# Performance work log

Hardware: AMD Instinct MI355X
Metric: run time of the kernel (lower is better)

The kernel has to match this reference:

```python
import jax, jax.numpy as jnp
import numpy as np

N = 4096          # nodes (single graph, batch=None)
E = 65536         # edges (avg degree 16)
C = 256           # hidden_channels
L = 3             # num_layers
H = 8             # attention heads
EPS = 1e-5        # batchnorm eps


def setup_inputs() -> dict:
    key = jax.random.key(0)
    ks = iter(jax.random.split(key, 64))
    s = 0.05
    d = {}
    d['x'] = jax.random.normal(next(ks), (N, 1), dtype=jnp.float32)
    d['edge_index'] = jax.random.randint(next(ks), (2, E), 0, N, dtype=jnp.int32)
    # input projection Linear(1, C)
    d['lin1_w'] = jax.random.normal(next(ks), (C, 1), dtype=jnp.float32) * s
    d['lin1_b'] = jnp.zeros((C,), dtype=jnp.float32)
    # GIN MLP: Linear(C,C) -> ReLU -> Linear(C,C), stacked over layers
    d['gin_w1'] = jax.random.normal(next(ks), (L, C, C), dtype=jnp.float32) * s
    d['gin_b1'] = jnp.zeros((L, C), dtype=jnp.float32)
    d['gin_w2'] = jax.random.normal(next(ks), (L, C, C), dtype=jnp.float32) * s
    d['gin_b2'] = jnp.zeros((L, C), dtype=jnp.float32)
    # MultiheadAttention projections
    for nm in ['attn_wq', 'attn_wk', 'attn_wv', 'attn_wo']:
        d[nm] = jax.random.normal(next(ks), (L, C, C), dtype=jnp.float32) * s
    for nm in ['attn_bq', 'attn_bk', 'attn_bv', 'attn_bo']:
        d[nm] = jnp.zeros((L, C), dtype=jnp.float32)
    # three BatchNorms per GPSConv layer
    for nm in ['bn1', 'bn2', 'bn3']:
        d[nm + '_g'] = jnp.ones((L, C), dtype=jnp.float32)
        d[nm + '_b'] = jnp.zeros((L, C), dtype=jnp.float32)
    # GPSConv feedforward: Linear(C, 2C) -> ReLU -> Linear(2C, C)
    d['mlp_w1'] = jax.random.normal(next(ks), (L, 2 * C, C), dtype=jnp.float32) * s
    d['mlp_b1'] = jnp.zeros((L, 2 * C), dtype=jnp.float32)
    d['mlp_w2'] = jax.random.normal(next(ks), (L, C, 2 * C), dtype=jnp.float32) * s
    d['mlp_b2'] = jnp.zeros((L, C), dtype=jnp.float32)
    return d


def _bn(v, g, b):
    # training-mode BatchNorm1d over the node dimension (biased variance)
    m = v.mean(0)
    var = v.var(0)
    return (v - m) * jax.lax.rsqrt(var + EPS) * g + b


def _gps_forward(x, edge_index, lin1_w, lin1_b, gin_w1, gin_b1, gin_w2, gin_b2,
                 attn_wq, attn_bq, attn_wk, attn_bk, attn_wv, attn_bv,
                 attn_wo, attn_bo, bn1_g, bn1_b, bn2_g, bn2_b, bn3_g, bn3_b,
                 mlp_w1, mlp_b1, mlp_w2, mlp_b2):
    h = x @ lin1_w.T + lin1_b                     # [N, C]
    src, dst = edge_index[0], edge_index[1]
    dh = C // H
    scale = 1.0 / jnp.sqrt(jnp.float32(dh))
    for l in range(L):
        xin = h
        # --- GIN branch: gather -> scatter-sum -> MLP ---
        agg = jax.ops.segment_sum(xin[src], dst, num_segments=N)   # [N, C]
        z = xin + agg                                               # eps=0
        z = jax.nn.relu(z @ gin_w1[l].T + gin_b1[l]) @ gin_w2[l].T + gin_b2[l]
        h1 = _bn(z + xin, bn1_g[l], bn1_b[l])
        # --- global multihead attention over all N nodes ---
        q = (xin @ attn_wq[l].T + attn_bq[l]).reshape(N, H, dh)
        k = (xin @ attn_wk[l].T + attn_bk[l]).reshape(N, H, dh)
        v = (xin @ attn_wv[l].T + attn_bv[l]).reshape(N, H, dh)
        scores = jnp.einsum('nhd,mhd->hnm', q, k) * scale           # [H, N, N]
        a = jax.nn.softmax(scores, axis=-1)
        o = jnp.einsum('hnm,mhd->nhd', a, v).reshape(N, C)
        o = o @ attn_wo[l].T + attn_bo[l]
        h2 = _bn(o + xin, bn2_g[l], bn2_b[l])
        # --- combine + feedforward ---
        s = h1 + h2
        m = jax.nn.relu(s @ mlp_w1[l].T + mlp_b1[l]) @ mlp_w2[l].T + mlp_b2[l]
        h = _bn(s + m, bn3_g[l], bn3_b[l])
    return h


def reference(x, edge_index, lin1_w, lin1_b, gin_w1, gin_b1, gin_w2, gin_b2,
              attn_wq, attn_bq, attn_wk, attn_bk, attn_wv, attn_bv,
              attn_wo, attn_bo, bn1_g, bn1_b, bn2_g, bn2_b, bn3_g, bn3_b,
              mlp_w1, mlp_b1, mlp_w2, mlp_b2):
    return _gps_forward(x, edge_index, lin1_w, lin1_b, gin_w1, gin_b1, gin_w2,
                        gin_b2, attn_wq, attn_bq, attn_wk, attn_bk, attn_wv,
                        attn_bv, attn_wo, attn_bo, bn1_g, bn1_b, bn2_g, bn2_b,
                        bn3_g, bn3_b, mlp_w1, mlp_b1, mlp_w2, mlp_b2)
```

## Files before the change

kernel.cpp:

```cpp
#include <hip/hip_runtime.h>

#define NN 4096
#define NE 65536
#define C 256
#define NL 3
#define NH 8
#define DH 32
#define EPS 1e-5f
#define SPLIT 4
#define KT8 (NN/128/SPLIT)
#define SR 512
#define ATTN_BLKS ((NN/128)*NH*SPLIT)
#define VS 136

typedef __bf16 bf16x8 __attribute__((ext_vector_type(8)));
typedef __bf16 bf16x4v __attribute__((ext_vector_type(4)));
typedef float f32x4 __attribute__((ext_vector_type(4)));
typedef short bf16x4s __attribute__((ext_vector_type(4)));

#define QSCALE (0.17677669529663687f * 1.4426950408889634f)

#define CC1 (C*C)
#define GS 72

__global__ __launch_bounds__(256) void prep_w(const float* __restrict__ s0,
        const float* __restrict__ s1, const float* __restrict__ s2,
        const float* __restrict__ s3, const float* __restrict__ s4,
        const float* __restrict__ s5, const float* __restrict__ s6,
        const float* __restrict__ s7, __bf16* __restrict__ dst) {
    int g = blockIdx.y;
    int i = (blockIdx.x*256 + threadIdx.x)*4;
    const float* src; int n;
    switch (g) {
        case 0: src=s0; n=3*CC1; break;
        case 1: src=s1; n=3*CC1; break;
        case 2: src=s2; n=3*CC1; break;
        case 3: src=s3; n=3*CC1; break;
        case 4: src=s4; n=3*CC1; break;
        case 5: src=s5; n=3*CC1; break;
        case 6: src=s6; n=6*CC1; break;
        default: src=s7; n=6*CC1; break;
    }
    if (i >= n) return;
    size_t off;
    if (g >= 2 && g <= 4) {
        int l = i >> 16, rem = i & (CC1-1);
        off = (size_t)(6 + 3*l + (g-2))*CC1 + rem;
    } else {
        size_t base = (g==0) ? 0 : (g==1) ? 3*(size_t)CC1 : (g==5) ? 15*(size_t)CC1
                    : (g==6) ? 18*(size_t)CC1 : 24*(size_t)CC1;
        off = base + i;
    }
    float4 t = *(const float4*)(src + i);
    bf16x4v o = {(__bf16)t.x, (__bf16)t.y, (__bf16)t.z, (__bf16)t.w};
    *(bf16x4v*)(dst + off) = o;
}

__global__ __launch_bounds__(256) void lin1_kernel(const float* __restrict__ x,
        const float* __restrict__ w, const float* __restrict__ b,
        __bf16* __restrict__ out) {
    int n = blockIdx.x, c = threadIdx.x;
    out[(size_t)n*C + c] = (__bf16)(x[n]*w[c] + b[c]);
}

__global__ __launch_bounds__(256) void hist_kernel(const int* __restrict__ ei,
        int* __restrict__ cnt) {
    int e = blockIdx.x*256 + threadIdx.x;
    atomicAdd(&cnt[ei[NE + e]], 1);
}

__global__ __launch_bounds__(256) void scan_kernel(const int* __restrict__ cnt,
        int* __restrict__ rowptr, int* __restrict__ cursor) {
    __shared__ int tot[256];
    __shared__ int pre[257];
    int t = threadIdx.x;
    int base = t*16;
    int local[16];
    int s = 0;
    #pragma unroll
    for (int i = 0; i < 16; i++) { local[i] = s; s += cnt[base+i]; }
    tot[t] = s;
    __syncthreads();
    if (t == 0) {
        int acc = 0;
        for (int i = 0; i < 256; i++) { pre[i] = acc; acc += tot[i]; }
        pre[256] = acc;
    }
    __syncthreads();
    int off = pre[t];
    #pragma unroll
    for (int i = 0; i < 16; i++) {
        rowptr[base+i] = off + local[i];
        cursor[base+i] = off + local[i];
    }
    if (t == 0) rowptr[NN] = pre[256];
}

__global__ __launch_bounds__(256) void fill_kernel(const int* __restrict__ ei,
        int* __restrict__ cursor, int* __restrict__ eidsrc) {
    int e = blockIdx.x*256 + threadIdx.x;
    int dst = ei[NE + e], src = ei[e];
    int pos = atomicAdd(&cursor[dst], 1);
    eidsrc[pos] = src;
}

template<int QKV, int BN, int COMB>
__device__ __forceinline__ void gemm_core(int bm, int bn,
        const __bf16* A, const float* A2f, const __bf16* A2b, const __bf16* W,
        const float* b0, const float* b1, const float* b2,
        const __bf16* add1, const __bf16* add2,
        __bf16* out, __bf16* vt, float* stats,
        const float* coefs,
        const float* st1, const float* g1, const float* bb1,
        const float* st2, const float* g2, const float* bb2,
        const float* lsum,
        int K, int Nout, int relu, __bf16* As, __bf16* Ws) {
    int tid = threadIdx.x;
    int wave = tid >> 6, lane = tid & 63;
    int ln = lane & 15, quad = lane >> 4;
    int row = tid >> 2, kseg = (tid & 3) * 16;
    f32x4 acc[4] = {};
    for (int k0 = 0; k0 < K; k0 += 64) {
        __syncthreads();
        {
            bf16x8 a0, a1;
            if constexpr (COMB) {
                int rowg = bm + row;
                int head = (k0 + kseg) >> 5;
                float w[SPLIT];
                float tot = 0.f;
                #pragma unroll
                for (int zz = 0; zz < SPLIT; zz++) {
                    w[zz] = lsum[((size_t)zz*NH + head)*NN + rowg];
                    tot += w[zz];
                }
                float inv = 1.0f / tot;
                float v[16] = {};
                #pragma unroll
                for (int zz = 0; zz < SPLIT; zz++) {
                    const __bf16* p = &A[((size_t)zz*NN + rowg)*C + k0 + kseg];
                    bf16x8 x0 = *(const bf16x8*)p, x1 = *(const bf16x8*)(p + 8);
                    #pragma unroll
                    for (int j = 0; j < 8; j++) {
                        v[j]   += w[zz]*(float)x0[j];
                        v[8+j] += w[zz]*(float)x1[j];
                    }
                }
                #pragma unroll
                for (int j = 0; j < 8; j++) {
                    a0[j] = (__bf16)(v[j]*inv);
                    a1[j] = (__bf16)(v[8+j]*inv);
                }
            } else {
                const __bf16* ap = &A[(size_t)(bm+row)*K + k0 + kseg];
                a0 = *(const bf16x8*)ap;
                a1 = *(const bf16x8*)(ap + 8);
                if constexpr (BN == 1) {
                    const __bf16* p = &A2b[(size_t)(bm+row)*K + k0 + kseg];
                    bf16x8 z0 = *(const bf16x8*)p;
                    bf16x8 z1v = *(const bf16x8*)(p + 8);
                    float sc1[16], sh1[16], sc2[16], sh2[16];
                    #pragma unroll
                    for (int i = 0; i < 4; i++) {
                        *(float4*)&sc1[i*4] = *(const float4*)&coefs[k0 + kseg + i*4];
                        *(float4*)&sh1[i*4] = *(const float4*)&coefs[C + k0 + kseg + i*4];
                        *(float4*)&sc2[i*4] = *(const float4*)&coefs[2*C + k0 + kseg + i*4];
                        *(float4*)&sh2[i*4] = *(const float4*)&coefs[3*C + k0 + kseg + i*4];
                    }
                    #pragma unroll
                    for (int j = 0; j < 8; j++) {
                        a0[j] = (__bf16)((float)a0[j]*sc1[j] + sh1[j]
                                       + (float)z0[j]*sc2[j] + sh2[j]);
                        a1[j] = (__bf16)((float)a1[j]*sc1[8+j] + sh1[8+j]
                                       + (float)z1v[j]*sc2[8+j] + sh2[8+j]);
                    }
                } else if (A2f) {
                    const float* p = &A2f[(size_t)(bm+row)*K + k0 + kseg];
                    float4 t0 = *(const float4*)p;
                    float4 t1 = *(const float4*)(p+4);
                    float4 t2 = *(const float4*)(p+8);
                    float4 t3 = *(const float4*)(p+12);
                    a0[0]=(__bf16)((float)a0[0]+t0.x); a0[1]=(__bf16)((float)a0[1]+t0.y);
                    a0[2]=(__bf16)((float)a0[2]+t0.z); a0[3]=(__bf16)((float)a0[3]+t0.w);
                    a0[4]=(__bf16)((float)a0[4]+t1.x); a0[5]=(__bf16)((float)a0[5]+t1.y);
                    a0[6]=(__bf16)((float)a0[6]+t1.z); a0[7]=(__bf16)((float)a0[7]+t1.w);
                    a1[0]=(__bf16)((float)a1[0]+t2.x); a1[1]=(__bf16)((float)a1[1]+t2.y);
                    a1[2]=(__bf16)((float)a1[2]+t2.z); a1[3]=(__bf16)((float)a1[3]+t2.w);
                    a1[4]=(__bf16)((float)a1[4]+t3.x); a1[5]=(__bf16)((float)a1[5]+t3.y);
                    a1[6]=(__bf16)((float)a1[6]+t3.z); a1[7]=(__bf16)((float)a1[7]+t3.w);
                }
            }
            *(bf16x8*)&As[row*GS + kseg]     = a0;
            *(bf16x8*)&As[row*GS + kseg + 8] = a1;
            const __bf16* wp = &W[(size_t)(bn+row)*K + k0 + kseg];
            *(bf16x8*)&Ws[row*GS + kseg]     = *(const bf16x8*)wp;
            *(bf16x8*)&Ws[row*GS + kseg + 8] = *(const bf16x8*)(wp + 8);
        }
        __syncthreads();
        #pragma unroll
        for (int kt2 = 0; kt2 < 2; kt2++) {
            bf16x8 bfr = *(const bf16x8*)&Ws[(wave*16+ln)*GS + kt2*32 + quad*8];
            #pragma unroll
            for (int i = 0; i < 4; i++) {
                bf16x8 afr = *(const bf16x8*)&As[(i*16+ln)*GS + kt2*32 + quad*8];
                acc[i] = __builtin_amdgcn_mfma_f32_16x16x32_bf16(afr, bfr, acc[i], 0, 0, 0);
            }
        }
    }
    int col = bn + wave*16 + ln;
    if constexpr (QKV) {
        float bsv = col < 256 ? b0[col] : (col < 512 ? b1[col-256] : b2[col-512]);
        if (col < 512) {
            float osc = col < 256 ? (float)QSCALE : 1.0f;
            #pragma unroll
            for (int i = 0; i < 4; i++)
                #pragma unroll
                for (int rr = 0; rr < 4; rr++)
                    out[(size_t)(bm + i*16 + quad*4 + rr)*SR + col] =
                        (__bf16)((acc[i][rr] + bsv) * osc);
        } else {
            int vrow = col - 512;
            #pragma unroll
            for (int i = 0; i < 4; i++) {
                bf16x4v pk = {(__bf16)(acc[i][0]+bsv), (__bf16)(acc[i][1]+bsv),
                              (__bf16)(acc[i][2]+bsv), (__bf16)(acc[i][3]+bsv)};
                *(bf16x4v*)&vt[(size_t)vrow*NN + bm + i*16 + quad*4] = pk;
            }
        }
        return;
    }
    float bsv = b0[col];
    float sc1 = 0.f, sh1 = 0.f, sc2 = 0.f, sh2 = 0.f;
    if constexpr (BN == 2) {
        float m1 = st1[col]*(1.f/NN);
        sc1 = rsqrtf(st1[C+col]*(1.f/NN) - m1*m1 + EPS) * g1[col];
        sh1 = bb1[col] - m1*sc1;
        float m2 = st2[col]*(1.f/NN);
        sc2 = rsqrtf(st2[C+col]*(1.f/NN) - m2*m2 + EPS) * g2[col];
        sh2 = bb2[col] - m2*sc2;
    }
    float ssum = 0.f, ssq = 0.f;
    #pragma unroll
    for (int i = 0; i < 4; i++) {
        #pragma unroll
        for (int rr = 0; rr < 4; rr++) {
            int rw = bm + i*16 + quad*4 + rr;
            float vv = acc[i][rr] + bsv;
            if (relu) vv = fmaxf(vv, 0.f);
            size_t idx = (size_t)rw*Nout + col;
            if constexpr (BN == 2) {
                vv += (float)add1[idx]*sc1 + sh1 + (float)add2[idx]*sc2 + sh2;
            } else {
                if (add1) vv += (float)add1[idx];
                if (add2) vv += (float)add2[idx];
            }
            out[idx] = (__bf16)vv;
            ssum += vv; ssq += vv*vv;
        }
    }
    if (stats) {
        ssum += __shfl_xor(ssum, 16); ssum += __shfl_xor(ssum, 32);
        ssq  += __shfl_xor(ssq, 16);  ssq  += __shfl_xor(ssq, 32);
        if (quad == 0) {
            atomicAdd(&stats[col], ssum);
            atomicAdd(&stats[Nout + col], ssq);
        }
    }
}

__device__ __forceinline__ void attn_body(int t, const __bf16* __restrict__ qk,
        const __bf16* __restrict__ vt, __bf16* __restrict__ opart,
        float* __restrict__ lsum, __bf16* lds) {
    int z = t >> 8, head = (t >> 5) & 7, qb = (t & 31) * 128;
    int hb = head * DH;
    int tid = threadIdx.x;
    int wave = tid >> 6, lane = tid & 63;
    int ln = lane & 15, quad = lane >> 4;
    __bf16* Kb0 = lds;
    __bf16* Kb1 = lds + 4608;
    __bf16* Vb0 = lds + 9216;
    __bf16* Vb1 = lds + 9216 + 32*VS;

    bf16x8 qf[2];
    #pragma unroll
    for (int g = 0; g < 2; g++)
        qf[g] = *(const bf16x8*)&qk[(size_t)(qb + wave*32 + g*16 + ln)*SR + hb + quad*8];

    f32x4 ot[2][2] = {};
    f32x4 la[2] = {};
    const bf16x4s ones = {(short)0x3F80, (short)0x3F80, (short)0x3F80, (short)0x3F80};

    int srow = tid >> 1, sseg = (tid & 1) * 16;
    int vd = tid >> 3, vseg = (tid & 7) * 16;
    int kt0 = z * KT8;
    {
        const __bf16* kp = &qk[(size_t)(kt0*128 + srow)*SR + 256 + hb + sseg];
        *(bf16x8*)&Kb0[srow*36 + sseg]     = *(const bf16x8*)kp;
        *(bf16x8*)&Kb0[srow*36 + sseg + 8] = *(const bf16x8*)(kp + 8);
        const __bf16* vp = &vt[(size_t)(hb + vd)*NN + kt0*128 + vseg];
        *(bf16x8*)&Vb0[vd*VS + vseg]     = *(const bf16x8*)vp;
        *(bf16x8*)&Vb0[vd*VS + vseg + 8] = *(const bf16x8*)(vp + 8);
    }
    for (int i = 0; i < KT8; i++) {
        int kb = (kt0 + i) * 128;
        __bf16* Kc = (i & 1) ? Kb1 : Kb0;
        __bf16* Kn = (i & 1) ? Kb0 : Kb1;
        __bf16* Vc = (i & 1) ? Vb1 : Vb0;
        __bf16* Vn = (i & 1) ? Vb0 : Vb1;
        __syncthreads();
        bf16x8 nk0, nk1, nv0, nv1;
        bool hasNext = (i + 1 < KT8);
        if (hasNext) {
            const __bf16* kp = &qk[(size_t)(kb + 128 + srow)*SR + 256 + hb + sseg];
            nk0 = *(const bf16x8*)kp;
            nk1 = *(const bf16x8*)(kp + 8);
            const __bf16* vp = &vt[(size_t)(hb + vd)*NN + kb + 128 + vseg];
            nv0 = *(const bf16x8*)vp;
            nv1 = *(const bf16x8*)(vp + 8);
        }
        #pragma unroll
        for (int pr = 0; pr < 4; pr++) {
            bf16x8 kf0 = *(const bf16x8*)&Kc[((pr*2+0)*16+ln)*36 + quad*8];
            bf16x8 kf1 = *(const bf16x8*)&Kc[((pr*2+1)*16+ln)*36 + quad*8];
            bf16x4s vf[2][2];
            #pragma unroll
            for (int s = 0; s < 2; s++)
                #pragma unroll
                for (int h = 0; h < 2; h++)
                    vf[s][h] = *(const bf16x4s*)&Vc[(h*16+ln)*VS + (pr*2+s)*16 + quad*4];
            f32x4 zz = {0.f,0.f,0.f,0.f};
            f32x4 st00 = __builtin_amdgcn_mfma_f32_16x16x32_bf16(kf0, qf[0], zz, 0, 0, 0);
            f32x4 st10 = __builtin_amdgcn_mfma_f32_16x16x32_bf16(kf0, qf[1], zz, 0, 0, 0);
            f32x4 st01 = __builtin_amdgcn_mfma_f32_16x16x32_bf16(kf1, qf[0], zz, 0, 0, 0);
            f32x4 st11 = __builtin_amdgcn_mfma_f32_16x16x32_bf16(kf1, qf[1], zz, 0, 0, 0);
            union { __bf16 b[4]; bf16x4s s; } pf00, pf01, pf10, pf11;
            #pragma unroll
            for (int rr = 0; rr < 4; rr++) {
                pf00.b[rr] = (__bf16)__builtin_amdgcn_exp2f(st00[rr]);
                pf01.b[rr] = (__bf16)__builtin_amdgcn_exp2f(st01[rr]);
                pf10.b[rr] = (__bf16)__builtin_amdgcn_exp2f(st10[rr]);
                pf11.b[rr] = (__bf16)__builtin_amdgcn_exp2f(st11[rr]);
            }
            ot[0][0] = __builtin_amdgcn_mfma_f32_16x16x16bf16_1k(vf[0][0], pf00.s, ot[0][0], 0, 0, 0);
            ot[0][1] = __builtin_amdgcn_mfma_f32_16x16x16bf16_1k(vf[0][1], pf00.s, ot[0][1], 0, 0, 0);
            ot[1][0] = __builtin_amdgcn_mfma_f32_16x16x16bf16_1k(vf[0][0], pf10.s, ot[1][0], 0, 0, 0);
            ot[1][1] = __builtin_amdgcn_mfma_f32_16x16x16bf16_1k(vf[0][1], pf10.s, ot[1][1], 0, 0, 0);
            la[0]    = __builtin_amdgcn_mfma_f32_16x16x16bf16_1k(ones,     pf00.s, la[0],    0, 0, 0);
            la[1]    = __builtin_amdgcn_mfma_f32_16x16x16bf16_1k(ones,     pf10.s, la[1],    0, 0, 0);
            ot[0][0] = __builtin_amdgcn_mfma_f32_16x16x16bf16_1k(vf[1][0], pf01.s, ot[0][0], 0, 0, 0);
            ot[0][1] = __builtin_amdgcn_mfma_f32_16x16x16bf16_1k(vf[1][1], pf01.s, ot[0][1], 0, 0, 0);
            ot[1][0] = __builtin_amdgcn_mfma_f32_16x16x16bf16_1k(vf[1][0], pf11.s, ot[1][0], 0, 0, 0);
            ot[1][1] = __builtin_amdgcn_mfma_f32_16x16x16bf16_1k(vf[1][1], pf11.s, ot[1][1], 0, 0, 0);
            la[0]    = __builtin_amdgcn_mfma_f32_16x16x16bf16_1k(ones,     pf01.s, la[0],    0, 0, 0);
            la[1]    = __builtin_amdgcn_mfma_f32_16x16x16bf16_1k(ones,     pf11.s, la[1],    0, 0, 0);
        }
        if (hasNext) {
            *(bf16x8*)&Kn[srow*36 + sseg]     = nk0;
            *(bf16x8*)&Kn[srow*36 + sseg + 8] = nk1;
            *(bf16x8*)&Vn[vd*VS + vseg]     = nv0;
            *(bf16x8*)&Vn[vd*VS + vseg + 8] = nv1;
        }
    }
    #pragma unroll
    for (int g = 0; g < 2; g++) {
        float l_ = la[g][0];
        float inv = 1.0f / l_;
        int qrow = qb + wave*32 + g*16 + ln;
        #pragma unroll
        for (int h = 0; h < 2; h++) {
            bf16x4v pk = {(__bf16)(ot[g][h][0]*inv), (__bf16)(ot[g][h][1]*inv),
                          (__bf16)(ot[g][h][2]*inv), (__bf16)(ot[g][h][3]*inv)};
            *(bf16x4v*)&opart[((size_t)z*NN + qrow)*C + hb + h*16 + quad*4] = pk;
        }
        if (quad == 0)
            lsum[((size_t)z*NH + head)*NN + qrow] = l_;
    }
}

__global__ __launch_bounds__(256) void qkv_agg_kernel(const __bf16* __restrict__ Hb,
        const __bf16* __restrict__ Wqkv, const float* __restrict__ bq,
        const float* __restrict__ bk, const float* __restrict__ bv,
        __bf16* __restrict__ qkout, __bf16* __restrict__ vtout,
        const int* __restrict__ rowptr, const int* __restrict__ eidsrc,
        float* __restrict__ agg) {
    __shared__ __bf16 lds[9216];
    int bx = blockIdx.x;
    if (bx < 768) {
        gemm_core<1,0,0>((bx & 63)*64, (bx >> 6)*64, Hb, nullptr, nullptr, Wqkv,
                bq, bk, bv, nullptr, nullptr, qkout, vtout, nullptr,
                nullptr, nullptr, nullptr, nullptr, nullptr, nullptr, nullptr,
                nullptr, C, 768, 0, lds, lds + 4608);
        return;
    }
    int tid = threadIdx.x;
    int wave = tid >> 6, lane = tid & 63;
    int node = (bx - 768)*4 + wave;
    int beg = rowptr[node], end = rowptr[node+1];
    float s0 = 0.f, s1 = 0.f, s2 = 0.f, s3 = 0.f;
    for (int e = beg; e < end; e++) {
        int src = eidsrc[e];
        bf16x4v hv = *(const bf16x4v*)&Hb[(size_t)src*C + lane*4];
        s0 += (float)hv[0]; s1 += (float)hv[1];
        s2 += (float)hv[2]; s3 += (float)hv[3];
    }
    float4 o = {s0, s1, s2, s3};
    *(float4*)&agg[(size_t)node*C + lane*4] = o;
}

__global__ __launch_bounds__(256) void gin1_attn_kernel(const __bf16* __restrict__ Hb,
        const float* __restrict__ agg, const __bf16* __restrict__ gw1,
        const float* __restrict__ gb1, __bf16* __restrict__ t1,
        const __bf16* __restrict__ qk, const __bf16* __restrict__ vt,
        __bf16* __restrict__ opart, float* __restrict__ lsum) {
    __shared__ __bf16 lds[17920];
    int bx = blockIdx.x;
    if (bx < 256) {
        gemm_core<0,0,0>((bx >> 2)*64, (bx & 3)*64, Hb, agg, nullptr, gw1,
                gb1, nullptr, nullptr, nullptr, nullptr, t1, nullptr, nullptr,
                nullptr, nullptr, nullptr, nullptr, nullptr, nullptr, nullptr,
                nullptr, C, C, 1, lds, lds + 4608);
        return;
    }
    attn_body(bx - 256, qk, vt, opart, lsum, lds);
}

__global__ __launch_bounds__(256) void gin2_proj_kernel(const __bf16* __restrict__ t1,
        const __bf16* __restrict__ gw2, const float* __restrict__ gb2,
        const __bf16* __restrict__ Hb, __bf16* __restrict__ z1, float* __restrict__ st1,
        const __bf16* __restrict__ opart, const float* __restrict__ lsum,
        const __bf16* __restrict__ wop, const float* __restrict__ lbo,
        __bf16* __restrict__ z2, float* __restrict__ st2) {
    __shared__ __bf16 lds[9216];
    int bx = blockIdx.x;
    if (bx < 256) {
        gemm_core<0,0,0>((bx >> 2)*64, (bx & 3)*64, t1, nullptr, nullptr, gw2,
                gb2, nullptr, nullptr, Hb, nullptr, z1, nullptr, st1,
                nullptr, nullptr, nullptr, nullptr, nullptr, nullptr, nullptr,
                nullptr, C, C, 0, lds, lds + 4608);
        return;
    }
    int t = bx - 256;
    gemm_core<0,0,1>((t >> 2)*64, (t & 3)*64, opart, nullptr, nullptr, wop,
            lbo, nullptr, nullptr, Hb, nullptr, z2, nullptr, st2,
            nullptr, nullptr, nullptr, nullptr, nullptr, nullptr, nullptr,
            lsum, C, C, 0, lds, lds + 4608);
}

__global__ __launch_bounds__(256) void ff1_kernel(const __bf16* __restrict__ z1,
        const __bf16* __restrict__ z2, const __bf16* __restrict__ mw1,
        const float* __restrict__ lmb1, __bf16* __restrict__ hidden,
        const float* __restrict__ st1, const float* __restrict__ g1,
        const float* __restrict__ bb1, const float* __restrict__ st2,
        const float* __restrict__ g2, const float* __restrict__ bb2) {
    __shared__ __bf16 lds[9216];
    __shared__ float coefs[4*C];
    int tid = threadIdx.x;
    {
        float m = st1[tid]*(1.f/NN);
        float var = st1[C+tid]*(1.f/NN) - m*m;
        float s = rsqrtf(var + EPS) * g1[tid];
        coefs[tid] = s; coefs[C+tid] = bb1[tid] - m*s;
        m = st2[tid]*(1.f/NN);
        var = st2[C+tid]*(1.f/NN) - m*m;
        s = rsqrtf(var + EPS) * g2[tid];
        coefs[2*C+tid] = s; coefs[3*C+tid] = bb2[tid] - m*s;
    }
    int bx = blockIdx.x;
    gemm_core<0,1,0>((bx >> 3)*64, (bx & 7)*64, z1, nullptr, z2, mw1,
            lmb1, nullptr, nullptr, nullptr, nullptr, hidden, nullptr, nullptr,
            coefs, nullptr, nullptr, nullptr, nullptr, nullptr, nullptr,
            nullptr, C, 2*C, 1, lds, lds + 4608);
}

__global__ __launch_bounds__(256) void ff2_kernel(const __bf16* __restrict__ hidden,
        const __bf16* __restrict__ mw2, const float* __restrict__ lmb2,
        const __bf16* __restrict__ z1, const __bf16* __restrict__ z2,
        __bf16* __restrict__ zbuf3, float* __restrict__ st3,
        const float* __restrict__ st1, const float* __restrict__ g1,
        const float* __restrict__ bb1, const float* __restrict__ st2,
        const float* __restrict__ g2, const float* __restrict__ bb2) {
    __shared__ __bf16 lds[9216];
    int bx = blockIdx.x;
    gemm_core<0,2,0>((bx >> 2)*64, (bx & 3)*64, hidden, nullptr, nullptr, mw2,
            lmb2, nullptr, nullptr, z1, z2, zbuf3, nullptr, st3,
            nullptr, st1, g1, bb1, st2, g2, bb2,
            nullptr, 2*C, C, 0, lds, lds + 4608);
}

__global__ __launch_bounds__(256) void bn_apply_kernel(const __bf16* __restrict__ z,
        const float* __restrict__ stats, const float* __restrict__ g,
        const float* __restrict__ b, __bf16* __restrict__ outb,
        float* __restrict__ outf) {
    int idx4 = (blockIdx.x*256 + threadIdx.x) * 4;
    int c = idx4 & (C-1);
    bf16x4v zv = *(const bf16x4v*)&z[idx4];
    float4 st = *(const float4*)&stats[c];
    float4 sq = *(const float4*)&stats[C + c];
    float4 gv = *(const float4*)&g[c];
    float4 bv = *(const float4*)&b[c];
    float o[4];
    float m0 = st.x*(1.f/NN), m1 = st.y*(1.f/NN), m2 = st.z*(1.f/NN), m3 = st.w*(1.f/NN);
    o[0] = ((float)zv[0] - m0) * rsqrtf(sq.x*(1.f/NN) - m0*m0 + EPS) * gv.x + bv.x;
    o[1] = ((float)zv[1] - m1) * rsqrtf(sq.y*(1.f/NN) - m1*m1 + EPS) * gv.y + bv.y;
    o[2] = ((float)zv[2] - m2) * rsqrtf(sq.z*(1.f/NN) - m2*m2 + EPS) * gv.z + bv.z;
    o[3] = ((float)zv[3] - m3) * rsqrtf(sq.w*(1.f/NN) - m3*m3 + EPS) * gv.w + bv.w;
    if (outb) {
        bf16x4v ov = {(__bf16)o[0], (__bf16)o[1], (__bf16)o[2], (__bf16)o[3]};
        *(bf16x4v*)&outb[idx4] = ov;
    } else {
        float4 ov = {o[0], o[1], o[2], o[3]};
        *(float4*)&outf[idx4] = ov;
    }
}

extern "C" void kernel_launch(void* const* d_in, const int* in_sizes, int n_in,
                              void* d_out, int out_size, void* d_ws, size_t ws_size,
                              hipStream_t stream) {
    const float* x      = (const float*)d_in[0];
    const int*   ei     = (const int*)d_in[1];
    const float* lin1_w = (const float*)d_in[2];
    const float* lin1_b = (const float*)d_in[3];
    const float* gin_w1 = (const float*)d_in[4];
    const float* gin_b1 = (const float*)d_in[5];
    const float* gin_w2 = (const float*)d_in[6];
    const float* gin_b2 = (const float*)d_in[7];
    const float* wq = (const float*)d_in[8];
    const float* wk = (const float*)d_in[9];
    const float* wv = (const float*)d_in[10];
    const float* wo = (const float*)d_in[11];
    const float* bq = (const float*)d_in[12];
    const float* bk = (const float*)d_in[13];
    const float* bv = (const float*)d_in[14];
    const float* bo = (const float*)d_in[15];
    const float* bn1_g = (const float*)d_in[16];
    const float* bn1_b = (const float*)d_in[17];
    const float* bn2_g = (const float*)d_in[18];
    const float* bn2_b = (const float*)d_in[19];
    const float* bn3_g = (const float*)d_in[20];
    const float* bn3_b = (const float*)d_in[21];
    const float* mw1 = (const float*)d_in[22];
    const float* mb1 = (const float*)d_in[23];
    const float* mw2 = (const float*)d_in[24];
    const float* mb2 = (const float*)d_in[25];

    const size_t MB = 1u << 20;
    char* ws = (char*)d_ws;
    __bf16* Hb      = (__bf16*)(ws);
    __bf16* z1      = (__bf16*)(ws + 2*MB);
    __bf16* zbuf3   = (__bf16*)(ws + 4*MB);
    __bf16* z2      = (__bf16*)(ws + 6*MB);
    __bf16* t1      = (__bf16*)(ws + 8*MB);
    __bf16* QKbuf   = (__bf16*)(ws + 10*MB);
    __bf16* Vt      = (__bf16*)(ws + 14*MB);
    float*  agg     = (float*)(ws + 16*MB);
    __bf16* hiddenb = (__bf16*)(ws + 16*MB);
    __bf16* Opart   = (__bf16*)(ws + 20*MB);
    __bf16* Wb      = (__bf16*)(ws + 28*MB);
    float*  stats   = (float*)(ws + 32*MB);
    int*    cursor  = (int*)(ws + 32*MB + 64*1024);
    int*    rowptr  = (int*)(ws + 32*MB + 96*1024);
    int*    eidsrc  = (int*)(ws + 32*MB + 128*1024);
    float*  lsum    = (float*)(ws + 33*MB);

    dim3 blk(256);

    prep_w<<<dim3(384, 8), blk, 0, stream>>>(gin_w1, gin_w2, wq, wk, wv, wo, mw1, mw2, Wb);
    hipMemsetAsync(stats, 0, 9 * 2 * C * sizeof(float), stream);
    lin1_kernel<<<NN, blk, 0, stream>>>(x, lin1_w, lin1_b, Hb);
    hipMemsetAsync(cursor, 0, NN * sizeof(int), stream);
    hist_kernel<<<NE/256, blk, 0, stream>>>(ei, cursor);
    scan_kernel<<<1, blk, 0, stream>>>(cursor, rowptr, cursor);
    fill_kernel<<<NE/256, blk, 0, stream>>>(ei, cursor, eidsrc);

    for (int l = 0; l < NL; l++) {
        const __bf16* gw1b = Wb + (size_t)l*CC1;
        const __bf16* gw2b = Wb + (size_t)(3+l)*CC1;
        const __bf16* wqkv = Wb + (size_t)(6+3*l)*CC1;
        const __bf16* wop  = Wb + (size_t)(15+l)*CC1;
        const __bf16* mw1p = Wb + (size_t)(18+2*l)*CC1;
        const __bf16* mw2p = Wb + (size_t)(24+2*l)*CC1;
        const float* gb1 = gin_b1 + (size_t)l*C;
        const float* gb2 = gin_b2 + (size_t)l*C;
        const float* lbq = bq + (size_t)l*C;
        const float* lbk = bk + (size_t)l*C;
        const float* lbv = bv + (size_t)l*C;
        const float* lbo = bo + (size_t)l*C;
        const float* lmb1 = mb1 + (size_t)l*2*C;
        const float* lmb2 = mb2 + (size_t)l*C;
        float* st1 = stats + (size_t)l*3*2*C;
        float* st2 = st1 + 2*C;
        float* st3 = st2 + 2*C;
        const float* g1v = bn1_g + (size_t)l*C; const float* b1v = bn1_b + (size_t)l*C;
        const float* g2v = bn2_g + (size_t)l*C; const float* b2v = bn2_b + (size_t)l*C;

        qkv_agg_kernel<<<768 + NN/4, blk, 0, stream>>>(Hb, wqkv, lbq, lbk, lbv,
                QKbuf, Vt, rowptr, eidsrc, agg);
        gin1_attn_kernel<<<256 + ATTN_BLKS, blk, 0, stream>>>(Hb, agg,
                gw1b, gb1, t1, QKbuf, Vt, Opart, lsum);
        gin2_proj_kernel<<<512, blk, 0, stream>>>(t1, gw2b, gb2, Hb, z1, st1,
                Opart, lsum, wop, lbo, z2, st2);
        ff1_kernel<<<512, blk, 0, stream>>>(z1, z2, mw1p, lmb1, hiddenb,
                st1, g1v, b1v, st2, g2v, b2v);
        ff2_kernel<<<256, blk, 0, stream>>>(hiddenb, mw2p, lmb2, z1, z2,
                zbuf3, st3, st1, g1v, b1v, st2, g2v, b2v);
        if (l == NL-1)
            bn_apply_kernel<<<NN/4, blk, 0, stream>>>(zbuf3, st3,
                    bn3_g + (size_t)l*C, bn3_b + (size_t)l*C, nullptr, (float*)d_out);
        else
            bn_apply_kernel<<<NN/4, blk, 0, stream>>>(zbuf3, st3,
                    bn3_g + (size_t)l*C, bn3_b + (size_t)l*C, Hb, nullptr);
    }
}
```

Before: 432.4 us.

## Store K head-major, split Q buffer, halve attention KV split

```diff
diff --git a/kernel.cpp b/kernel.cpp
--- a/kernel.cpp
+++ b/kernel.cpp
@@ -7,9 +7,8 @@
 #define NH 8
 #define DH 32
 #define EPS 1e-5f
-#define SPLIT 4
+#define SPLIT 2
 #define KT8 (NN/128/SPLIT)
-#define SR 512
 #define ATTN_BLKS ((NN/128)*NH*SPLIT)
 #define VS 136
 
@@ -109,7 +108,7 @@
         const __bf16* A, const float* A2f, const __bf16* A2b, const __bf16* W,
         const float* b0, const float* b1, const float* b2,
         const __bf16* add1, const __bf16* add2,
-        __bf16* out, __bf16* vt, float* stats,
+        __bf16* out, __bf16* vt, __bf16* ktp, float* stats,
         const float* coefs,
         const float* st1, const float* g1, const float* bb1,
         const float* st2, const float* g2, const float* bb2,
@@ -210,14 +209,21 @@
     int col = bn + wave*16 + ln;
     if constexpr (QKV) {
         float bsv = col < 256 ? b0[col] : (col < 512 ? b1[col-256] : b2[col-512]);
-        if (col < 512) {
-            float osc = col < 256 ? (float)QSCALE : 1.0f;
+        if (col < 256) {
             #pragma unroll
             for (int i = 0; i < 4; i++)
                 #pragma unroll
                 for (int rr = 0; rr < 4; rr++)
-                    out[(size_t)(bm + i*16 + quad*4 + rr)*SR + col] =
-                        (__bf16)((acc[i][rr] + bsv) * osc);
+                    out[(size_t)(bm + i*16 + quad*4 + rr)*C + col] =
+                        (__bf16)((acc[i][rr] + bsv) * (float)QSCALE);
+        } else if (col < 512) {
+            int hd = (col-256) >> 5, dh = (col-256) & 31;
+            #pragma unroll
+            for (int i = 0; i < 4; i++)
+                #pragma unroll
+                for (int rr = 0; rr < 4; rr++)
+                    ktp[((size_t)hd*NN + bm + i*16 + quad*4 + rr)*DH + dh] =
+                        (__bf16)(acc[i][rr] + bsv);
         } else {
             int vrow = col - 512;
             #pragma unroll
@@ -268,10 +274,10 @@
     }
 }
 
-__device__ __forceinline__ void attn_body(int t, const __bf16* __restrict__ qk,
-        const __bf16* __restrict__ vt, __bf16* __restrict__ opart,
-        float* __restrict__ lsum, __bf16* lds) {
-    int z = t >> 8, head = (t >> 5) & 7, qb = (t & 31) * 128;
+__device__ __forceinline__ void attn_body(int t, const __bf16* __restrict__ qbuf,
+        const __bf16* __restrict__ kt, const __bf16* __restrict__ vt,
+        __bf16* __restrict__ opart, float* __restrict__ lsum, __bf16* lds) {
+    int head = t & 7, z = t >> 8, qb = ((t >> 3) & 31) * 128;
     int hb = head * DH;
     int tid = threadIdx.x;
     int wave = tid >> 6, lane = tid & 63;
@@ -284,7 +290,7 @@
     bf16x8 qf[2];
     #pragma unroll
     for (int g = 0; g < 2; g++)
-        qf[g] = *(const bf16x8*)&qk[(size_t)(qb + wave*32 + g*16 + ln)*SR + hb + quad*8];
+        qf[g] = *(const bf16x8*)&qbuf[(size_t)(qb + wave*32 + g*16 + ln)*C + hb + quad*8];
 
     f32x4 ot[2][2] = {};
     f32x4 la[2] = {};
@@ -293,8 +299,9 @@
     int srow = tid >> 1, sseg = (tid & 1) * 16;
     int vd = tid >> 3, vseg = (tid & 7) * 16;
     int kt0 = z * KT8;
+    const __bf16* kbase = &kt[(size_t)head*NN*DH];
     {
-        const __bf16* kp = &qk[(size_t)(kt0*128 + srow)*SR + 256 + hb + sseg];
+        const __bf16* kp = &kbase[(size_t)(kt0*128 + srow)*DH + sseg];
         *(bf16x8*)&Kb0[srow*36 + sseg]     = *(const bf16x8*)kp;
         *(bf16x8*)&Kb0[srow*36 + sseg + 8] = *(const bf16x8*)(kp + 8);
         const __bf16* vp = &vt[(size_t)(hb + vd)*NN + kt0*128 + vseg];
@@ -311,7 +318,7 @@
         bf16x8 nk0, nk1, nv0, nv1;
         bool hasNext = (i + 1 < KT8);
         if (hasNext) {
-            const __bf16* kp = &qk[(size_t)(kb + 128 + srow)*SR + 256 + hb + sseg];
+            const __bf16* kp = &kbase[(size_t)(kb + 128 + srow)*DH + sseg];
             nk0 = *(const bf16x8*)kp;
             nk1 = *(const bf16x8*)(kp + 8);
             const __bf16* vp = &vt[(size_t)(hb + vd)*NN + kb + 128 + vseg];
@@ -380,14 +387,15 @@
 __global__ __launch_bounds__(256) void qkv_agg_kernel(const __bf16* __restrict__ Hb,
         const __bf16* __restrict__ Wqkv, const float* __restrict__ bq,
         const float* __restrict__ bk, const float* __restrict__ bv,
-        __bf16* __restrict__ qkout, __bf16* __restrict__ vtout,
+        __bf16* __restrict__ qout, __bf16* __restrict__ ktout,
+        __bf16* __restrict__ vtout,
         const int* __restrict__ rowptr, const int* __restrict__ eidsrc,
         float* __restrict__ agg) {
     __shared__ __bf16 lds[9216];
     int bx = blockIdx.x;
     if (bx < 768) {
         gemm_core<1,0,0>((bx & 63)*64, (bx >> 6)*64, Hb, nullptr, nullptr, Wqkv,
-                bq, bk, bv, nullptr, nullptr, qkout, vtout, nullptr,
+                bq, bk, bv, nullptr, nullptr, qout, vtout, ktout, nullptr,
                 nullptr, nullptr, nullptr, nullptr, nullptr, nullptr, nullptr,
                 nullptr, C, 768, 0, lds, lds + 4608);
         return;
@@ -410,7 +418,8 @@
 __global__ __launch_bounds__(256) void gin1_attn_kernel(const __bf16* __restrict__ Hb,
         const float* __restrict__ agg, const __bf16* __restrict__ gw1,
         const float* __restrict__ gb1, __bf16* __restrict__ t1,
-        const __bf16* __restrict__ qk, const __bf16* __restrict__ vt,
+        const __bf16* __restrict__ qbuf, const __bf16* __restrict__ kt,
+        const __bf16* __restrict__ vt,
         __bf16* __restrict__ opart, float* __restrict__ lsum) {
     __shared__ __bf16 lds[17920];
     int bx = blockIdx.x;
@@ -418,10 +427,10 @@
         gemm_core<0,0,0>((bx >> 2)*64, (bx & 3)*64, Hb, agg, nullptr, gw1,
                 gb1, nullptr, nullptr, nullptr, nullptr, t1, nullptr, nullptr,
                 nullptr, nullptr, nullptr, nullptr, nullptr, nullptr, nullptr,
-                nullptr, C, C, 1, lds, lds + 4608);
+                nullptr, nullptr, C, C, 1, lds, lds + 4608);
         return;
     }
-    attn_body(bx - 256, qk, vt, opart, lsum, lds);
+    attn_body(bx - 256, qbuf, kt, vt, opart, lsum, lds);
 }
 
 __global__ __launch_bounds__(256) void gin2_proj_kernel(const __bf16* __restrict__ t1,
@@ -434,14 +443,14 @@
     int bx = blockIdx.x;
     if (bx < 256) {
         gemm_core<0,0,0>((bx >> 2)*64, (bx & 3)*64, t1, nullptr, nullptr, gw2,
-                gb2, nullptr, nullptr, Hb, nullptr, z1, nullptr, st1,
+                gb2, nullptr, nullptr, Hb, nullptr, z1, nullptr, nullptr, st1,
                 nullptr, nullptr, nullptr, nullptr, nullptr, nullptr, nullptr,
                 nullptr, C, C, 0, lds, lds + 4608);
         return;
     }
     int t = bx - 256;
     gemm_core<0,0,1>((t >> 2)*64, (t & 3)*64, opart, nullptr, nullptr, wop,
-            lbo, nullptr, nullptr, Hb, nullptr, z2, nullptr, st2,
+            lbo, nullptr, nullptr, Hb, nullptr, z2, nullptr, nullptr, st2,
             nullptr, nullptr, nullptr, nullptr, nullptr, nullptr, nullptr,
             lsum, C, C, 0, lds, lds + 4608);
 }
@@ -468,7 +477,7 @@
     int bx = blockIdx.x;
     gemm_core<0,1,0>((bx >> 3)*64, (bx & 7)*64, z1, nullptr, z2, mw1,
             lmb1, nullptr, nullptr, nullptr, nullptr, hidden, nullptr, nullptr,
-            coefs, nullptr, nullptr, nullptr, nullptr, nullptr, nullptr,
+            nullptr, coefs, nullptr, nullptr, nullptr, nullptr, nullptr, nullptr,
             nullptr, C, 2*C, 1, lds, lds + 4608);
 }
 
@@ -482,7 +491,7 @@
     __shared__ __bf16 lds[9216];
     int bx = blockIdx.x;
     gemm_core<0,2,0>((bx >> 2)*64, (bx & 3)*64, hidden, nullptr, nullptr, mw2,
-            lmb2, nullptr, nullptr, z1, z2, zbuf3, nullptr, st3,
+            lmb2, nullptr, nullptr, z1, z2, zbuf3, nullptr, nullptr, st3,
             nullptr, st1, g1, bb1, st2, g2, bb2,
             nullptr, 2*C, C, 0, lds, lds + 4608);
 }
@@ -550,7 +559,8 @@
     __bf16* zbuf3   = (__bf16*)(ws + 4*MB);
     __bf16* z2      = (__bf16*)(ws + 6*MB);
     __bf16* t1      = (__bf16*)(ws + 8*MB);
-    __bf16* QKbuf   = (__bf16*)(ws + 10*MB);
+    __bf16* Qbuf    = (__bf16*)(ws + 10*MB);
+    __bf16* Ktb     = (__bf16*)(ws + 12*MB);
     __bf16* Vt      = (__bf16*)(ws + 14*MB);
     float*  agg     = (float*)(ws + 16*MB);
     __bf16* hiddenb = (__bf16*)(ws + 16*MB);
@@ -594,9 +604,9 @@
         const float* g2v = bn2_g + (size_t)l*C; const float* b2v = bn2_b + (size_t)l*C;
 
         qkv_agg_kernel<<<768 + NN/4, blk, 0, stream>>>(Hb, wqkv, lbq, lbk, lbv,
-                QKbuf, Vt, rowptr, eidsrc, agg);
+                Qbuf, Ktb, Vt, rowptr, eidsrc, agg);
         gin1_attn_kernel<<<256 + ATTN_BLKS, blk, 0, stream>>>(Hb, agg,
-                gw1b, gb1, t1, QKbuf, Vt, Opart, lsum);
+                gw1b, gb1, t1, Qbuf, Ktb, Vt, Opart, lsum);
         gin2_proj_kernel<<<512, blk, 0, stream>>>(t1, gw2b, gb2, Hb, z1, st1,
                 Opart, lsum, wop, lbo, z2, st2);
         ff1_kernel<<<512, blk, 0, stream>>>(z1, z2, mw1p, lmb1, hiddenb,
```

Measured after the change: 435.0 us. No clear change (+0.6%).
